# Performance work log

Hardware: AMD Instinct MI355X
Metric: run time of the kernel (lower is better)

Reference implementation:

```python
import jax, jax.numpy as jnp
import numpy as np

B, C, H, W = 1, 64, 128, 128
OUT = 512          # target resolution per side
Q = OUT * OUT      # 262144 query points
D_IN = C * 9 + 2 + 2  # 580: unfolded feat + rel_coord + rel_cell


def setup_inputs() -> dict:
    key = jax.random.key(0)
    k1, k2, k3 = jax.random.split(key, 3)
    feat = jax.random.normal(k1, (B, C, H, W), jnp.float32)
    coord = jax.random.uniform(k2, (B, Q, 2), jnp.float32, -1.0, 1.0)
    cell = jnp.full((B, Q, 2), 2.0 / OUT, jnp.float32)
    imnet_w = jax.random.normal(k3, (D_IN, 3), jnp.float32) * 0.02
    imnet_b = jnp.zeros((3,), jnp.float32)
    return {"feat": feat, "coord": coord, "cell": cell,
            "imnet_w": imnet_w, "imnet_b": imnet_b}


def _unfold3(feat):
    # F.unfold(feat, 3, padding=1).view(B, C*9, H, W): channel order c*9 + (di*3+dj)
    b, c, h, w = feat.shape
    p = jnp.pad(feat, ((0, 0), (0, 0), (1, 1), (1, 1)))
    patches = jnp.stack([p[:, :, di:di + h, dj:dj + w]
                         for di in range(3) for dj in range(3)], axis=2)
    return patches.reshape(b, c * 9, h, w)


def _nearest_idx(g, size):
    # grid_sample nearest, align_corners=False: idx = floor((g+1)*size/2), clipped
    return jnp.clip(jnp.floor((g + 1.0) * size / 2.0).astype(jnp.int32), 0, size - 1)


def reference(feat, coord, cell, imnet_w, imnet_b):
    bsz, _, h, w = feat.shape
    featU = _unfold3(feat)                         # (B, C*9, H, W)
    rx, ry = 1.0 / h, 1.0 / w                      # 2/size/2
    eps_shift = 1e-6
    scale = jnp.asarray([h, w], feat.dtype)
    # pixel-center coords (make_coord): -1 + (2i+1)/n
    cx = (-1.0 + (2.0 * jnp.arange(h) + 1.0) / h).astype(feat.dtype)
    cy = (-1.0 + (2.0 * jnp.arange(w) + 1.0) / w).astype(feat.dtype)
    rel_cell = cell * scale
    b_idx = jnp.arange(bsz)[:, None]
    preds, areas = [], []
    for vx in (-1, 1):
        for vy in (-1, 1):
            shift = jnp.asarray([vx * rx + eps_shift, vy * ry + eps_shift], feat.dtype)
            c_ = jnp.clip(coord + shift, -1 + 1e-6, 1 - 1e-6)
            ih = _nearest_idx(c_[..., 0], h)       # (B, Q)
            iw = _nearest_idx(c_[..., 1], w)
            q_feat = featU[b_idx, :, ih, iw]       # (B, Q, C*9)
            q_coord = jnp.stack([cx[ih], cy[iw]], axis=-1)  # (B, Q, 2)
            rel = (coord - q_coord) * scale
            inp = jnp.concatenate([q_feat, rel, rel_cell], axis=-1)  # (B, Q, 580)
            preds.append(inp @ imnet_w + imnet_b)  # (B, Q, 3)
            areas.append(jnp.abs(rel[..., 0] * rel[..., 1]) + 1e-9)
    tot = areas[0] + areas[1] + areas[2] + areas[3]
    # local_ensemble: swap diagonal areas
    areas = [areas[3], areas[2], areas[1], areas[0]]
    ret = sum(p * (a / tot)[..., None] for p, a in zip(preds, areas))
    return ret
```

## Files before the change

kernel.cpp:

```cpp
#include <hip/hip_runtime.h>

constexpr int Hc = 128, Wc = 128, Cc = 64;
constexpr int Qc = 512 * 512;

constexpr int PIX_PER_BLK = 16;
constexpr int CGRP = 16;
constexpr int CPER = Cc / CGRP;

__global__ __launch_bounds__(256) void conv3x3_S(const float* __restrict__ feat,
                                                 const float* __restrict__ wgt,
                                                 float* __restrict__ S) {
    __shared__ float ws[576 * 3];
    for (int i = threadIdx.x; i < 576 * 3; i += 256) ws[i] = wgt[i];

    __shared__ float part[CGRP][PIX_PER_BLK][3];

    int px = threadIdx.x & (PIX_PER_BLK - 1);
    int cg = threadIdx.x >> 4;
    int pix = blockIdx.x * PIX_PER_BLK + px;
    int y = pix >> 7;
    int x = pix & 127;

    __syncthreads();

    float a0 = 0.f, a1 = 0.f, a2 = 0.f;
    const int c0 = cg * CPER;
#pragma unroll
    for (int ci = 0; ci < CPER; ++ci) {
        int c = c0 + ci;
        const float* fc = feat + c * Hc * Wc;
        const float* wr = ws + c * 27;
#pragma unroll
        for (int di = 0; di < 3; ++di) {
            int yy = y + di - 1;
            bool yok = (unsigned)yy < (unsigned)Hc;
#pragma unroll
            for (int dj = 0; dj < 3; ++dj) {
                int xx = x + dj - 1;
                bool ok = yok && ((unsigned)xx < (unsigned)Wc);
                float v = ok ? fc[yy * Wc + xx] : 0.f;
                const float* wk = wr + (di * 3 + dj) * 3;
                a0 = fmaf(v, wk[0], a0);
                a1 = fmaf(v, wk[1], a1);
                a2 = fmaf(v, wk[2], a2);
            }
        }
    }

    part[cg][px][0] = a0;
    part[cg][px][1] = a1;
    part[cg][px][2] = a2;
    __syncthreads();

#pragma unroll
    for (int step = CGRP / 2; step > 0; step >>= 1) {
        if (cg < step) {
            part[cg][px][0] += part[cg + step][px][0];
            part[cg][px][1] += part[cg + step][px][1];
            part[cg][px][2] += part[cg + step][px][2];
        }
        __syncthreads();
    }

    if (cg == 0) {
        float4 o;
        o.x = part[0][px][0];
        o.y = part[0][px][1];
        o.z = part[0][px][2];
        o.w = 0.f;
        *reinterpret_cast<float4*>(S + pix * 4) = o;
    }
}

__global__ __launch_bounds__(256) void liif_query(const float* __restrict__ coord,
                                                  const float* __restrict__ cell,
                                                  const float* __restrict__ wgt,
                                                  const float* __restrict__ bias,
                                                  const float* __restrict__ S,
                                                  float* __restrict__ out) {
    int t = blockIdx.x * 256 + threadIdx.x;
    int q0 = t * 2;

    float4 co = *reinterpret_cast<const float4*>(coord + q0 * 2);
    float4 ce = *reinterpret_cast<const float4*>(cell + q0 * 2);

    float wx0 = wgt[576 * 3 + 0], wx1 = wgt[576 * 3 + 1], wx2 = wgt[576 * 3 + 2];
    float wy0 = wgt[577 * 3 + 0], wy1 = wgt[577 * 3 + 1], wy2 = wgt[577 * 3 + 2];
    float wc0 = wgt[578 * 3 + 0], wc1 = wgt[578 * 3 + 1], wc2 = wgt[578 * 3 + 2];
    float wd0 = wgt[579 * 3 + 0], wd1 = wgt[579 * 3 + 1], wd2 = wgt[579 * 3 + 2];
    float b0 = bias[0], b1 = bias[1], b2 = bias[2];

    constexpr float SHN = (float)(-1.0 / 128.0 + 1e-6);
    constexpr float SHP = (float)( 1.0 / 128.0 + 1e-6);
    constexpr float CLO = (float)(-1.0 + 1e-6);
    constexpr float CHI = (float)( 1.0 - 1e-6);

    float res[6];
#pragma unroll
    for (int k = 0; k < 2; ++k) {
        float cox = k ? co.z : co.x;
        float coy = k ? co.w : co.y;
        float rcx = (k ? ce.z : ce.x) * 128.0f;
        float rcy = (k ? ce.w : ce.y) * 128.0f;

        float pr[4][3];
        float area[4];
#pragma unroll
        for (int s = 0; s < 4; ++s) {
            float sx = (s < 2) ? SHN : SHP;
            float sy = (s & 1) ? SHP : SHN;
            float cx_ = fminf(fmaxf(cox + sx, CLO), CHI);
            float cy_ = fminf(fmaxf(coy + sy, CLO), CHI);
            int ih = (int)floorf((cx_ + 1.0f) * 64.0f);
            ih = min(max(ih, 0), 127);
            int iw = (int)floorf((cy_ + 1.0f) * 64.0f);
            iw = min(max(iw, 0), 127);
            float qx = -1.0f + (float)(2 * ih + 1) * (1.0f / 128.0f);
            float qy = -1.0f + (float)(2 * iw + 1) * (1.0f / 128.0f);
            float relx = (cox - qx) * 128.0f;
            float rely = (coy - qy) * 128.0f;

            float4 sv = *reinterpret_cast<const float4*>(S + (ih * 128 + iw) * 4);
            pr[s][0] = sv.x + relx * wx0 + rely * wy0 + rcx * wc0 + rcy * wd0 + b0;
            pr[s][1] = sv.y + relx * wx1 + rely * wy1 + rcx * wc1 + rcy * wd1 + b1;
            pr[s][2] = sv.z + relx * wx2 + rely * wy2 + rcx * wc2 + rcy * wd2 + b2;
            area[s] = fabsf(relx * rely) + 1e-9f;
        }

        float tot = area[0] + area[1] + area[2] + area[3];
        float inv = 1.0f / tot;
        float g0 = area[3] * inv, g1 = area[2] * inv, g2 = area[1] * inv, g3 = area[0] * inv;

        res[k * 3 + 0] = pr[0][0] * g0 + pr[1][0] * g1 + pr[2][0] * g2 + pr[3][0] * g3;
        res[k * 3 + 1] = pr[0][1] * g0 + pr[1][1] * g1 + pr[2][1] * g2 + pr[3][1] * g3;
        res[k * 3 + 2] = pr[0][2] * g0 + pr[1][2] * g1 + pr[2][2] * g2 + pr[3][2] * g3;
    }

    float2* op = reinterpret_cast<float2*>(out + q0 * 3);
    op[0] = make_float2(res[0], res[1]);
    op[1] = make_float2(res[2], res[3]);
    op[2] = make_float2(res[4], res[5]);
}

extern "C" void kernel_launch(void* const* d_in, const int* in_sizes, int n_in,
                              void* d_out, int out_size, void* d_ws, size_t ws_size,
                              hipStream_t stream) {
    const float* feat  = (const float*)d_in[0];
    const float* coord = (const float*)d_in[1];
    const float* cell  = (const float*)d_in[2];
    const float* wgt   = (const float*)d_in[3];
    const float* bias  = (const float*)d_in[4];
    float* out = (float*)d_out;
    float* S   = (float*)d_ws;

    conv3x3_S<<<(Hc * Wc) / PIX_PER_BLK, 256, 0, stream>>>(feat, wgt, S);
    liif_query<<<Qc / 512, 256, 0, stream>>>(coord, cell, wgt, bias, S, out);
}
```

Measured before the change: 16.34 us.

## Pack conv table to fp16 and stage it in shared memory for queries

The per-pixel 3-channel conv result is stored as packed fp16 (8 bytes) instead of a float4, halving the table to 128 KB. The query kernel copies the whole table into dynamic LDS per block and gathers from LDS instead of global/L2. It runs 256 blocks with 4 queries per thread. The aim is cheaper random gathers, at the cost of fp16 rounding error, a full 128 KB copy per block, one block per CU, and uncoalesced scalar output stores.

Result: slower. 22.87 us (+40.0%).

```diff
diff --git a/kernel.cpp b/kernel.cpp
--- a/kernel.cpp
+++ b/kernel.cpp
@@ -1,4 +1,5 @@
 #include <hip/hip_runtime.h>
+#include <hip/hip_fp16.h>
 
 constexpr int Hc = 128, Wc = 128, Cc = 64;
 constexpr int Qc = 512 * 512;
@@ -7,9 +8,13 @@
 constexpr int CGRP = 16;
 constexpr int CPER = Cc / CGRP;
 
+constexpr int QBLK = 256;
+constexpr int QPT = Qc / (QBLK * 256);
+constexpr int TAB_BYTES = Hc * Wc * 8;
+
 __global__ __launch_bounds__(256) void conv3x3_S(const float* __restrict__ feat,
                                                  const float* __restrict__ wgt,
-                                                 float* __restrict__ S) {
+                                                 uint2* __restrict__ Sp) {
     __shared__ float ws[576 * 3];
     for (int i = threadIdx.x; i < 576 * 3; i += 256) ws[i] = wgt[i];
 
@@ -63,12 +68,13 @@
     }
 
     if (cg == 0) {
-        float4 o;
-        o.x = part[0][px][0];
-        o.y = part[0][px][1];
-        o.z = part[0][px][2];
-        o.w = 0.f;
-        *reinterpret_cast<float4*>(S + pix * 4) = o;
+        unsigned short u0 = __half_as_ushort(__float2half_rn(part[0][px][0]));
+        unsigned short u1 = __half_as_ushort(__float2half_rn(part[0][px][1]));
+        unsigned short u2 = __half_as_ushort(__float2half_rn(part[0][px][2]));
+        uint2 o;
+        o.x = (unsigned)u0 | ((unsigned)u1 << 16);
+        o.y = (unsigned)u2;
+        Sp[pix] = o;
     }
 }
 
@@ -76,13 +82,24 @@
                                                   const float* __restrict__ cell,
                                                   const float* __restrict__ wgt,
                                                   const float* __restrict__ bias,
-                                                  const float* __restrict__ S,
+                                                  const uint2* __restrict__ Sp,
                                                   float* __restrict__ out) {
-    int t = blockIdx.x * 256 + threadIdx.x;
-    int q0 = t * 2;
+    extern __shared__ uint2 tab[];
 
-    float4 co = *reinterpret_cast<const float4*>(coord + q0 * 2);
-    float4 ce = *reinterpret_cast<const float4*>(cell + q0 * 2);
+    const int qbase = blockIdx.x * (QPT * 256) + threadIdx.x;
+    float2 cos_[QPT], ces_[QPT];
+#pragma unroll
+    for (int r = 0; r < QPT; ++r) {
+        int q = qbase + r * 256;
+        cos_[r] = *reinterpret_cast<const float2*>(coord + q * 2);
+        ces_[r] = *reinterpret_cast<const float2*>(cell + q * 2);
+    }
+
+    {
+        const uint4* src = reinterpret_cast<const uint4*>(Sp);
+        uint4* dst = reinterpret_cast<uint4*>(tab);
+        for (int i = threadIdx.x; i < TAB_BYTES / 16; i += 256) dst[i] = src[i];
+    }
 
     float wx0 = wgt[576 * 3 + 0], wx1 = wgt[576 * 3 + 1], wx2 = wgt[576 * 3 + 2];
     float wy0 = wgt[577 * 3 + 0], wy1 = wgt[577 * 3 + 1], wy2 = wgt[577 * 3 + 2];
@@ -90,18 +107,19 @@
     float wd0 = wgt[579 * 3 + 0], wd1 = wgt[579 * 3 + 1], wd2 = wgt[579 * 3 + 2];
     float b0 = bias[0], b1 = bias[1], b2 = bias[2];
 
+    __syncthreads();
+
     constexpr float SHN = (float)(-1.0 / 128.0 + 1e-6);
     constexpr float SHP = (float)( 1.0 / 128.0 + 1e-6);
     constexpr float CLO = (float)(-1.0 + 1e-6);
     constexpr float CHI = (float)( 1.0 - 1e-6);
 
-    float res[6];
 #pragma unroll
-    for (int k = 0; k < 2; ++k) {
-        float cox = k ? co.z : co.x;
-        float coy = k ? co.w : co.y;
-        float rcx = (k ? ce.z : ce.x) * 128.0f;
-        float rcy = (k ? ce.w : ce.y) * 128.0f;
+    for (int r = 0; r < QPT; ++r) {
+        int q = qbase + r * 256;
+        float cox = cos_[r].x, coy = cos_[r].y;
+        float rcx = ces_[r].x * 128.0f;
+        float rcy = ces_[r].y * 128.0f;
 
         float pr[4][3];
         float area[4];
@@ -120,10 +138,13 @@
             float relx = (cox - qx) * 128.0f;
             float rely = (coy - qy) * 128.0f;
 
-            float4 sv = *reinterpret_cast<const float4*>(S + (ih * 128 + iw) * 4);
-            pr[s][0] = sv.x + relx * wx0 + rely * wy0 + rcx * wc0 + rcy * wd0 + b0;
-            pr[s][1] = sv.y + relx * wx1 + rely * wy1 + rcx * wc1 + rcy * wd1 + b1;
-            pr[s][2] = sv.z + relx * wx2 + rely * wy2 + rcx * wc2 + rcy * wd2 + b2;
+            uint2 sv = tab[ih * 128 + iw];
+            float2 s01 = __half22float2(*reinterpret_cast<const __half2*>(&sv.x));
+            float s2 = __half2float(__ushort_as_half((unsigned short)(sv.y & 0xffffu)));
+
+            pr[s][0] = s01.x + relx * wx0 + rely * wy0 + rcx * wc0 + rcy * wd0 + b0;
+            pr[s][1] = s01.y + relx * wx1 + rely * wy1 + rcx * wc1 + rcy * wd1 + b1;
+            pr[s][2] = s2    + relx * wx2 + rely * wy2 + rcx * wc2 + rcy * wd2 + b2;
             area[s] = fabsf(relx * rely) + 1e-9f;
         }
 
@@ -131,15 +152,10 @@
         float inv = 1.0f / tot;
         float g0 = area[3] * inv, g1 = area[2] * inv, g2 = area[1] * inv, g3 = area[0] * inv;
 
-        res[k * 3 + 0] = pr[0][0] * g0 + pr[1][0] * g1 + pr[2][0] * g2 + pr[3][0] * g3;
-        res[k * 3 + 1] = pr[0][1] * g0 + pr[1][1] * g1 + pr[2][1] * g2 + pr[3][1] * g3;
-        res[k * 3 + 2] = pr[0][2] * g0 + pr[1][2] * g1 + pr[2][2] * g2 + pr[3][2] * g3;
+        out[q * 3 + 0] = pr[0][0] * g0 + pr[1][0] * g1 + pr[2][0] * g2 + pr[3][0] * g3;
+        out[q * 3 + 1] = pr[0][1] * g0 + pr[1][1] * g1 + pr[2][1] * g2 + pr[3][1] * g3;
+        out[q * 3 + 2] = pr[0][2] * g0 + pr[1][2] * g1 + pr[2][2] * g2 + pr[3][2] * g3;
     }
-
-    float2* op = reinterpret_cast<float2*>(out + q0 * 3);
-    op[0] = make_float2(res[0], res[1]);
-    op[1] = make_float2(res[2], res[3]);
-    op[2] = make_float2(res[4], res[5]);
 }
 
 extern "C" void kernel_launch(void* const* d_in, const int* in_sizes, int n_in,
@@ -151,8 +167,12 @@
     const float* wgt   = (const float*)d_in[3];
     const float* bias  = (const float*)d_in[4];
     float* out = (float*)d_out;
-    float* S   = (float*)d_ws;
+    uint2* Sp  = (uint2*)d_ws;
 
-    conv3x3_S<<<(Hc * Wc) / PIX_PER_BLK, 256, 0, stream>>>(feat, wgt, S);
-    liif_query<<<Qc / 512, 256, 0, stream>>>(coord, cell, wgt, bias, S, out);
+    static_assert(TAB_BYTES == 131072, "table size");
+    hipFuncSetAttribute((const void*)liif_query,
+                        hipFuncAttributeMaxDynamicSharedMemorySize, TAB_BYTES);
+
+    conv3x3_S<<<(Hc * Wc) / PIX_PER_BLK, 256, 0, stream>>>(feat, wgt, Sp);
+    liif_query<<<QBLK, 256, TAB_BYTES, stream>>>(coord, cell, wgt, bias, Sp, out);
 }
```
